# Optimization experiments

Measured on AMD Instinct MI355X. Metric: run time of the kernel, lower is better.

Reference implementation:

```python
import jax, jax.numpy as jnp
import numpy as np

V, D, NL, K, B, L, FF = 32000, 512, 4, 32, 2, 1024, 2048


def _ln(x, g, b, eps=1e-5):
    m = jnp.mean(x, axis=-1, keepdims=True)
    v = jnp.mean((x - m) ** 2, axis=-1, keepdims=True)
    return (x - m) * jax.lax.rsqrt(v + eps) * g + b


def setup_inputs() -> dict:
    key = jax.random.key(0)
    ks = jax.random.split(key, 16)
    s = 0.02
    n = lambda k, shape: jax.random.normal(k, shape, jnp.float32) * s
    inp = {
        "tokens": jax.random.randint(ks[0], (B, L), 0, V),
        "embed": n(ks[1], (V, D)),
        "ln1_g": jnp.ones((NL, D)), "ln1_b": jnp.zeros((NL, D)),
        "cp_w1": n(ks[2], (NL, D, D)), "cp_b1": jnp.zeros((NL, D)),
        "cp_w2": n(ks[3], (NL, D, K)), "cp_b2": jnp.zeros((NL, K)),
        "pos_scale": 0.5 * jnp.ones((NL,)), "content_scale": 0.5 * jnp.ones((NL,)),
        "val_w": n(ks[4], (NL, D, D)), "val_b": jnp.zeros((NL, D)),
        "oln_g": jnp.ones((NL, D)), "oln_b": jnp.zeros((NL, D)),
        "out_w": n(ks[5], (NL, D, D)), "out_b": jnp.zeros((NL, D)),
        "ln2_g": jnp.ones((NL, D)), "ln2_b": jnp.zeros((NL, D)),
        "ffn_w1": n(ks[6], (NL, D, FF)), "ffn_b1": jnp.zeros((NL, FF)),
        "ffn_w2": n(ks[7], (NL, FF, D)), "ffn_b2": jnp.zeros((NL, D)),
        "no_g": jnp.ones((D,)), "no_b": jnp.zeros((D,)),
        "head_b": jnp.zeros((V,)),
    }
    return inp


def _forward(tokens, embed, ln1_g, ln1_b, cp_w1, cp_b1, cp_w2, cp_b2,
             pos_scale, content_scale, val_w, val_b, oln_g, oln_b, out_w, out_b,
             ln2_g, ln2_b, ffn_w1, ffn_b1, ffn_w2, ffn_b2, no_g, no_b, head_b):
    Bn, Ln = tokens.shape
    Kn = cp_b2.shape[1]
    # fixed positional phases (register_buffer in torch)
    freqs = 1.0 / 10000.0 ** (jnp.arange(Kn, dtype=jnp.float32) / Kn)
    pos_phase = jnp.arange(Ln, dtype=jnp.float32)[:, None] * freqs[None, :]  # [L,K]
    inv_norm = 1.0 / jnp.sqrt(jnp.arange(1, Ln + 1, dtype=jnp.float32) * Kn)[None, :, None]
    h = embed[tokens]  # [B,L,D]
    for i in range(ln1_g.shape[0]):
        # --- DualAddressingPhasor on normed input ---
        x = _ln(h, ln1_g[i], ln1_b[i])
        cp = jnp.tanh(jnp.tanh(x @ cp_w1[i] + cp_b1[i]) @ cp_w2[i] + cp_b2[i]) * jnp.pi  # [B,L,K]
        tp = pos_scale[i] * pos_phase[None] + content_scale[i] * cp
        v = x @ val_w[i] + val_b[i]  # [B,L,D]
        c, s_ = jnp.cos(tp), jnp.sin(tp)  # [B,L,K]
        mem_r = jnp.cumsum(c[..., None] * v[:, :, None, :], axis=1)  # [B,L,K,D]
        mem_i = jnp.cumsum(s_[..., None] * v[:, :, None, :], axis=1)
        retrieved = (jnp.einsum('blkd,blk->bld', mem_r, c)
                     + jnp.einsum('blkd,blk->bld', mem_i, s_)) * inv_norm
        # phasor returns x + to_out(retrieved); block adds it back to h
        h = h + x + (_ln(retrieved, oln_g[i], oln_b[i]) @ out_w[i] + out_b[i])
        # --- FFN ---
        y = _ln(h, ln2_g[i], ln2_b[i])
        h = h + jax.nn.gelu(y @ ffn_w1[i] + ffn_b1[i], approximate=False) @ ffn_w2[i] + ffn_b2[i]
    # tied output head: head.weight = embed.weight
    return _ln(h, no_g, no_b) @ embed.T + head_b


def reference(tokens, embed, ln1_g, ln1_b, cp_w1, cp_b1, cp_w2, cp_b2,
              pos_scale, content_scale, val_w, val_b, oln_g, oln_b, out_w, out_b,
              ln2_g, ln2_b, ffn_w1, ffn_b1, ffn_w2, ffn_b2, no_g, no_b, head_b):
    return _forward(tokens, embed, ln1_g, ln1_b, cp_w1, cp_b1, cp_w2, cp_b2,
                    pos_scale, content_scale, val_w, val_b, oln_g, oln_b, out_w, out_b,
                    ln2_g, ln2_b, ffn_w1, ffn_b1, ffn_w2, ffn_b2, no_g, no_b, head_b)
```

## Files before the change

### kernel.cpp

```cpp
#include <hip/hip_runtime.h>
#include <hip/hip_bf16.h>
#include <math.h>

#define V_  32000
#define D_  512
#define NL_ 4
#define K_  32
#define B_  2
#define L_  1024
#define FF_ 2048
#define MR_ (B_ * L_)

typedef __bf16 bf16_t;
typedef __bf16 bf16x8 __attribute__((ext_vector_type(8)));
typedef float  f32x4  __attribute__((ext_vector_type(4)));

#define FLAG_TANH   1
#define FLAG_GELU   2
#define FLAG_INV    8
#define FLAG_CAUSAL 16
#define FLAG_TANHLO 32

#define GLDS(gsrc, ldst) \
  __builtin_amdgcn_global_load_lds( \
      (const __attribute__((address_space(1))) unsigned int*)(const void*)(gsrc), \
      (__attribute__((address_space(3))) unsigned int*)(void*)(ldst), 16, 0, 0)

__global__ void gather_kernel(const int* __restrict__ tokens,
                              const float* __restrict__ embed,
                              float* __restrict__ h) {
    int row = blockIdx.x;
    int t = tokens[row];
    const float4* src = (const float4*)(embed + (size_t)t * D_);
    float4* dst = (float4*)(h + (size_t)row * D_);
    dst[threadIdx.x] = src[threadIdx.x];
}

__global__ __launch_bounds__(256) void cvt_kernel(const float* __restrict__ in,
                                                  bf16_t* __restrict__ out) {
    size_t i = ((size_t)blockIdx.x * 256 + threadIdx.x) * 8;
    float4 f0 = ((const float4*)(in + i))[0];
    float4 f1 = ((const float4*)(in + i))[1];
    bf16x8 ov;
    ov[0] = (bf16_t)f0.x; ov[1] = (bf16_t)f0.y;
    ov[2] = (bf16_t)f0.z; ov[3] = (bf16_t)f0.w;
    ov[4] = (bf16_t)f1.x; ov[5] = (bf16_t)f1.y;
    ov[6] = (bf16_t)f1.z; ov[7] = (bf16_t)f1.w;
    *(bf16x8*)(out + i) = ov;
}

__global__ void bconcat_kernel(const float* __restrict__ a,
                               const float* __restrict__ b,
                               float* __restrict__ o) {
    int i = blockIdx.x, t = threadIdx.x;
    o[(size_t)i * 2 * D_ + t]       = a[(size_t)i * D_ + t];
    o[(size_t)i * 2 * D_ + D_ + t]  = b[(size_t)i * D_ + t];
}

__global__ __launch_bounds__(256) void ln_kernel(const float* __restrict__ in,
                                                 const float* __restrict__ g,
                                                 const float* __restrict__ b,
                                                 float* __restrict__ outf,
                                                 bf16_t* __restrict__ outb) {
    int row = blockIdx.x, tid = threadIdx.x;
    const float* rp = in + (size_t)row * D_;
    float v0 = rp[tid], v1 = rp[tid + 256];
    float s = v0 + v1, q = v0 * v0 + v1 * v1;
#pragma unroll
    for (int o = 32; o > 0; o >>= 1) {
        s += __shfl_down(s, o, 64);
        q += __shfl_down(q, o, 64);
    }
    __shared__ float ss[4], sq[4];
    if ((tid & 63) == 0) { ss[tid >> 6] = s; sq[tid >> 6] = q; }
    __syncthreads();
    float ts = ss[0] + ss[1] + ss[2] + ss[3];
    float tq = sq[0] + sq[1] + sq[2] + sq[3];
    float mean = ts * (1.0f / D_);
    float var = tq * (1.0f / D_) - mean * mean;
    float rstd = rsqrtf(var + 1e-5f);
    float o0 = (v0 - mean) * rstd * g[tid] + b[tid];
    float o1 = (v1 - mean) * rstd * g[tid + 256] + b[tid + 256];
    if (outf) {
        outf[(size_t)row * D_ + tid]       = o0;
        outf[(size_t)row * D_ + tid + 256] = o1;
    }
    if (outb) {
        outb[(size_t)row * D_ + tid]       = (bf16_t)o0;
        outb[(size_t)row * D_ + tid + 256] = (bf16_t)o1;
    }
}

__global__ __launch_bounds__(256) void tconv_kernel(const float* __restrict__ in,
                                                    bf16_t* __restrict__ out,
                                                    int R, int C,
                                                    size_t inz, size_t outz) {
    __shared__ float t[32][33];
    const float* ip = in + (size_t)blockIdx.z * inz;
    bf16_t* op = out + (size_t)blockIdx.z * outz;
    int r0 = blockIdx.y * 32, c0 = blockIdx.x * 32;
    int tx = threadIdx.x & 31, ty = threadIdx.x >> 5;
#pragma unroll
    for (int rr = 0; rr < 4; ++rr)
        t[ty + rr * 8][tx] = ip[(size_t)(r0 + ty + rr * 8) * C + c0 + tx];
    __syncthreads();
#pragma unroll
    for (int rr = 0; rr < 4; ++rr)
        op[(size_t)(c0 + ty + rr * 8) * R + r0 + tx] = (bf16_t)t[tx][ty + rr * 8];
}

template<int BM, int BN, int NBUF, bool BF32>
__global__ __launch_bounds__(256) void mgemm(
    const bf16_t* __restrict__ A, const void* __restrict__ Bp,
    const float* __restrict__ bias, const float* __restrict__ res1,
    const float* __restrict__ res2, float* __restrict__ Cf,
    bf16_t* __restrict__ Cb, int M, int N, int Kd, int flags,
    long long strA, long long strB, long long strC, int swz) {
    __shared__ bf16_t sA[NBUF][BM * 32];
    __shared__ bf16_t sB[NBUF][BN * 32];
    const int tid = threadIdx.x;
    const int wave = tid >> 6, lane = tid & 63;
    const int lrow = lane & 15, quad = lane >> 4;
    int bx = blockIdx.x, by = blockIdx.y;
    if (swz) {
        int gx = gridDim.x, gy = gridDim.y;
        int nwg = gx * gy;
        int lid = by * gx + bx;
        int q = nwg >> 3, r = nwg & 7;
        int xcd = lid & 7, slot = lid >> 3;
        int base = (xcd < r) ? xcd * (q + 1) : r * (q + 1) + (xcd - r) * q;
        int nid = base + slot;
        bx = nid / gy;
        by = nid - bx * gy;
    }
    const int m0 = by * BM, n0 = bx * BN;
    const int z = blockIdx.z;
    A += (size_t)z * strA;
    const bf16_t* Bb = (const bf16_t*)Bp + (BF32 ? 0 : (size_t)z * strB);
    const float*  Bf = (const float*)Bp  + (BF32 ? (size_t)z * strB : 0);
    constexpr int TM = BM / 32, TN = BN / 32;
    const int wm = (wave >> 1) * (BM / 2), wn = (wave & 1) * (BN / 2);
    f32x4 acc[TM][TN] = {};

    if constexpr (BF32) {
        for (int k0 = 0; k0 < Kd; k0 += 32) {
#pragma unroll
            for (int rb = 0; rb < BM / 64; ++rb) {
                int rowblk = wave * (BM / 64) + rb;
                int ml = rowblk * 16 + (lane >> 2);
                int qs = (lane & 3) ^ ((ml >> 1) & 3);
                GLDS(A + (size_t)(m0 + ml) * Kd + k0 + qs * 8, &sA[0][rowblk * 512]);
            }
#pragma unroll
            for (int rb = 0; rb < (BN * 4) / 256; ++rb) {
                int s = rb * 256 + tid;
                int nl = s >> 2, ql = s & 3;
                int qs = ql ^ ((nl >> 1) & 3);
                const float* src = Bf + (size_t)(n0 + nl) * Kd + k0 + qs * 8;
                float4 f0 = ((const float4*)src)[0];
                float4 f1 = ((const float4*)src)[1];
                bf16x8 ov;
                ov[0] = (bf16_t)f0.x; ov[1] = (bf16_t)f0.y;
                ov[2] = (bf16_t)f0.z; ov[3] = (bf16_t)f0.w;
                ov[4] = (bf16_t)f1.x; ov[5] = (bf16_t)f1.y;
                ov[6] = (bf16_t)f1.z; ov[7] = (bf16_t)f1.w;
                *(bf16x8*)(&sB[0][s * 8]) = ov;
            }
            __syncthreads();
            bf16x8 af[TM], bv[TN];
#pragma unroll
            for (int i = 0; i < TM; ++i) {
                int row = wm + i * 16 + lrow;
                af[i] = *(const bf16x8*)(&sA[0][(row * 4 + (quad ^ ((row >> 1) & 3))) * 8]);
            }
#pragma unroll
            for (int j = 0; j < TN; ++j) {
                int rown = wn + j * 16 + lrow;
                bv[j] = *(const bf16x8*)(&sB[0][(rown * 4 + (quad ^ ((rown >> 1) & 3))) * 8]);
            }
#pragma unroll
            for (int i = 0; i < TM; ++i)
#pragma unroll
                for (int j = 0; j < TN; ++j)
                    acc[i][j] = __builtin_amdgcn_mfma_f32_16x16x32_bf16(af[i], bv[j], acc[i][j], 0, 0, 0);
            __syncthreads();
        }
    } else {
        int kend = Kd;
        if (flags & FLAG_CAUSAL) { int ke = m0 + BM; kend = ke < Kd ? ke : Kd; }
        const int nk = kend >> 5;
        constexpr int NLD = BM / 64 + BN / 64;
        auto stage = [&](int t) {
            const int buf = t & (NBUF - 1);
            const int k0 = t << 5;
#pragma unroll
            for (int rb = 0; rb < BM / 64; ++rb) {
                int rowblk = wave * (BM / 64) + rb;
                int ml = rowblk * 16 + (lane >> 2);
                int qs = (lane & 3) ^ ((ml >> 1) & 3);
                GLDS(A + (size_t)(m0 + ml) * Kd + k0 + qs * 8, &sA[buf][rowblk * 512]);
            }
#pragma unroll
            for (int rb = 0; rb < BN / 64; ++rb) {
                int rowblk = wave * (BN / 64) + rb;
                int nl = rowblk * 16 + (lane >> 2);
                int qs = (lane & 3) ^ ((nl >> 1) & 3);
                GLDS(Bb + (size_t)(n0 + nl) * Kd + k0 + qs * 8, &sB[buf][rowblk * 512]);
            }
        };
        for (int t = 0; t < NBUF - 1 && t < nk; ++t) stage(t);
        for (int t = 0; t < nk; ++t) {
            const int nxt = t + NBUF - 1;
            if (nxt < nk) stage(nxt);
            const int issued_last = (nxt < nk) ? nxt : nk - 1;
            const int ahead = issued_last - t;
            switch (ahead) {
              case 0: asm volatile("s_waitcnt vmcnt(0)" ::: "memory"); break;
              case 1: asm volatile("s_waitcnt vmcnt(%0)" :: "n"(1 * NLD) : "memory"); break;
              case 2: asm volatile("s_waitcnt vmcnt(%0)" :: "n"(2 * NLD) : "memory"); break;
              default: asm volatile("s_waitcnt vmcnt(%0)" :: "n"(3 * NLD) : "memory"); break;
            }
            __builtin_amdgcn_s_barrier();
            const int buf = t & (NBUF - 1);
            const bf16_t* sAc = sA[buf];
            const bf16_t* sBc = sB[buf];
            bf16x8 af[TM], bv[TN];
#pragma unroll
            for (int i = 0; i < TM; ++i) {
                int row = wm + i * 16 + lrow;
                af[i] = *(const bf16x8*)(sAc + (row * 4 + (quad ^ ((row >> 1) & 3))) * 8);
            }
#pragma unroll
            for (int j = 0; j < TN; ++j) {
                int rown = wn + j * 16 + lrow;
                bv[j] = *(const bf16x8*)(sBc + (rown * 4 + (quad ^ ((rown >> 1) & 3))) * 8);
            }
#pragma unroll
            for (int i = 0; i < TM; ++i)
#pragma unroll
                for (int j = 0; j < TN; ++j)
                    acc[i][j] = __builtin_amdgcn_mfma_f32_16x16x32_bf16(af[i], bv[j], acc[i][j], 0, 0, 0);
            asm volatile("s_waitcnt lgkmcnt(0)" ::: "memory");
            __builtin_amdgcn_s_barrier();
        }
    }

    const size_t zo = (size_t)z * strC;
#pragma unroll
    for (int i = 0; i < TM; ++i) {
#pragma unroll
        for (int reg = 0; reg < 4; ++reg) {
            int m = m0 + wm + i * 16 + quad * 4 + reg;
            float rs = (flags & FLAG_INV) ? rsqrtf((float)(m + 1) * (float)K_) : 1.0f;
#pragma unroll
            for (int j = 0; j < TN; ++j) {
                int n = n0 + wn + j * 16 + lrow;
                float vv = acc[i][j][reg];
                if (bias) vv += bias[n];
                vv *= rs;
                if (flags & FLAG_TANH) vv = tanhf(vv);
                else if (flags & FLAG_GELU) vv = 0.5f * vv * (1.0f + erff(vv * 0.7071067811865476f));
                else if (flags & FLAG_TANHLO) { if (n < D_) vv = tanhf(vv); }
                size_t idx = zo + (size_t)m * N + n;
                if (res1) vv += res1[idx];
                if (res2) vv += res2[idx];
                if (Cf) Cf[idx] = vv;
                if (Cb) Cb[idx] = (bf16_t)vv;
            }
        }
    }
}

__global__ void phase_kernel(const float* __restrict__ t1,
                             const float* __restrict__ w2,
                             const float* __restrict__ b2,
                             const float* __restrict__ ps,
                             const float* __restrict__ cs,
                             int layer,
                             float* __restrict__ cbuf,
                             float* __restrict__ sbuf) {
    int row = blockIdx.x;
    int l = row & (L_ - 1);
    int tid = threadIdx.x;
    int k = tid & 31, hh = tid >> 5;
    const float* tr = t1 + (size_t)row * (2 * D_);
    float acc = 0.f;
    for (int d = hh * 256; d < hh * 256 + 256; ++d)
        acc = fmaf(tr[d], w2[d * K_ + k], acc);
    __shared__ float red[64];
    red[tid] = acc;
    __syncthreads();
    if (hh == 0) {
        float zz = red[k] + red[k + 32] + b2[k];
        float cp = tanhf(zz) * 3.14159265358979323846f;
        float freq = expf(-(float)k * (9.210340371976184f / (float)K_));
        float tp = ps[layer] * (float)l * freq + cs[layer] * cp;
        cbuf[(size_t)row * K_ + k] = cosf(tp);
        sbuf[(size_t)row * K_ + k] = sinf(tp);
    }
}

__global__ __launch_bounds__(256) void score_kernel(const float* __restrict__ cbuf,
                                                    const float* __restrict__ sbuf,
                                                    bf16_t* __restrict__ Ab) {
    int b = blockIdx.z;
    int l0 = blockIdx.y * 16, j0 = blockIdx.x * 16;
    if (j0 > l0) return;
    int tx = threadIdx.x, ty = threadIdx.y;
    int tid = ty * 16 + tx;
    __shared__ float Cl[16][33], Sl[16][33], Cj[16][33], Sj[16][33];
    const float* cb = cbuf + (size_t)b * L_ * K_;
    const float* sb = sbuf + (size_t)b * L_ * K_;
    for (int q = tid; q < 16 * 32; q += 256) {
        int rr = q >> 5, kk = q & 31;
        Cl[rr][kk] = cb[(size_t)(l0 + rr) * K_ + kk];
        Sl[rr][kk] = sb[(size_t)(l0 + rr) * K_ + kk];
        Cj[rr][kk] = cb[(size_t)(j0 + rr) * K_ + kk];
        Sj[rr][kk] = sb[(size_t)(j0 + rr) * K_ + kk];
    }
    __syncthreads();
    int l = l0 + ty, j = j0 + tx;
    float acc = 0.f;
#pragma unroll
    for (int kk = 0; kk < 32; ++kk)
        acc += Cl[ty][kk] * Cj[tx][kk] + Sl[ty][kk] * Sj[tx][kk];
    Ab[((size_t)b * L_ + l) * L_ + j] = (bf16_t)((j <= l) ? acc : 0.f);
}

extern "C" void kernel_launch(void* const* d_in, const int* in_sizes, int n_in,
                              void* d_out, int out_size, void* d_ws, size_t ws_size,
                              hipStream_t stream) {
    const int*   tokens        = (const int*)d_in[0];
    const float* embed         = (const float*)d_in[1];
    const float* ln1_g         = (const float*)d_in[2];
    const float* ln1_b         = (const float*)d_in[3];
    const float* cp_w1         = (const float*)d_in[4];
    const float* cp_b1         = (const float*)d_in[5];
    const float* cp_w2         = (const float*)d_in[6];
    const float* cp_b2         = (const float*)d_in[7];
    const float* pos_scale     = (const float*)d_in[8];
    const float* content_scale = (const float*)d_in[9];
    const float* val_w         = (const float*)d_in[10];
    const float* val_b         = (const float*)d_in[11];
    const float* oln_g         = (const float*)d_in[12];
    const float* oln_b         = (const float*)d_in[13];
    const float* out_w         = (const float*)d_in[14];
    const float* out_b         = (const float*)d_in[15];
    const float* ln2_g         = (const float*)d_in[16];
    const float* ln2_b         = (const float*)d_in[17];
    const float* ffn_w1        = (const float*)d_in[18];
    const float* ffn_b1        = (const float*)d_in[19];
    const float* ffn_w2        = (const float*)d_in[20];
    const float* ffn_b2        = (const float*)d_in[21];
    const float* no_g          = (const float*)d_in[22];
    const float* no_b          = (const float*)d_in[23];
    const float* head_b        = (const float*)d_in[24];
    float* out = (float*)d_out;

    float* h   = out;
    float* x   = h  + (size_t)MR_ * D_;
    float* t1v = x  + (size_t)MR_ * D_;
    float* r   = t1v + (size_t)MR_ * 2 * D_;
    float* cb  = r  + (size_t)MR_ * D_;
    float* sb  = cb + (size_t)MR_ * K_;
    bf16_t* x_bf  = (bf16_t*)(sb + (size_t)MR_ * K_);
    bf16_t* r_bf  = x_bf  + (size_t)MR_ * D_;
    bf16_t* y_bf  = r_bf  + (size_t)MR_ * D_;
    bf16_t* ff_bf = y_bf  + (size_t)MR_ * D_;
    bf16_t* sc_bf = ff_bf + (size_t)MR_ * FF_;
    bf16_t* vT_bf = sc_bf + (size_t)B_ * L_ * L_;
    bf16_t* wvT   = vT_bf + (size_t)B_ * D_ * L_;
    bf16_t* owT   = wvT   + (size_t)NL_ * 2 * D_ * D_;
    bf16_t* f1T   = owT   + (size_t)NL_ * D_ * D_;
    bf16_t* f2T   = f1T   + (size_t)NL_ * FF_ * D_;
    float*  b1v   = (float*)((((uintptr_t)(f2T + (size_t)NL_ * D_ * FF_)) + 15) & ~(uintptr_t)15);
    bf16_t* hn_bf = (bf16_t*)d_ws;
    bf16_t* emb_bf = hn_bf + (size_t)MR_ * D_;
    const bool big_ws =
        ws_size >= ((size_t)MR_ * D_ + (size_t)V_ * D_) * sizeof(bf16_t);

    gather_kernel<<<MR_, 128, 0, stream>>>(tokens, embed, h);

    tconv_kernel<<<dim3(16, 16, NL_), 256, 0, stream>>>(cp_w1, wvT, D_, D_, (size_t)D_ * D_, (size_t)2 * D_ * D_);
    tconv_kernel<<<dim3(16, 16, NL_), 256, 0, stream>>>(val_w, wvT + (size_t)D_ * D_, D_, D_, (size_t)D_ * D_, (size_t)2 * D_ * D_);
    bconcat_kernel<<<NL_, 512, 0, stream>>>(cp_b1, val_b, b1v);
    tconv_kernel<<<dim3(16, 16, NL_), 256, 0, stream>>>(out_w, owT, D_, D_, (size_t)D_ * D_, (size_t)D_ * D_);
    tconv_kernel<<<dim3(64, 16, NL_), 256, 0, stream>>>(ffn_w1, f1T, D_, FF_, (size_t)D_ * FF_, (size_t)D_ * FF_);
    tconv_kernel<<<dim3(16, 64, NL_), 256, 0, stream>>>(ffn_w2, f2T, FF_, D_, (size_t)FF_ * D_, (size_t)FF_ * D_);
    if (big_ws)
        cvt_kernel<<<(V_ * D_) / 2048, 256, 0, stream>>>(embed, emb_bf);

    for (int i = 0; i < NL_; ++i) {
        ln_kernel<<<MR_, 256, 0, stream>>>(h, ln1_g + i * D_, ln1_b + i * D_, x, x_bf);
        mgemm<64, 64, 4, false><<<dim3(16, 32, 1), 256, 0, stream>>>(
            x_bf, wvT + (size_t)i * 2 * D_ * D_, b1v + (size_t)i * 2 * D_,
            nullptr, nullptr, t1v, nullptr, MR_, 2 * D_, D_, FLAG_TANHLO, 0, 0, 0, 1);
        phase_kernel<<<MR_, 64, 0, stream>>>(
            t1v, cp_w2 + (size_t)i * D_ * K_, cp_b2 + i * K_,
            pos_scale, content_scale, i, cb, sb);
        tconv_kernel<<<dim3(16, 32, B_), 256, 0, stream>>>(
            t1v + D_, vT_bf, L_, 2 * D_, (size_t)L_ * 2 * D_, (size_t)D_ * L_);
        score_kernel<<<dim3(L_ / 16, L_ / 16, B_), dim3(16, 16), 0, stream>>>(cb, sb, sc_bf);
        mgemm<64, 64, 4, false><<<dim3(8, 16, B_), 256, 0, stream>>>(
            sc_bf, vT_bf, nullptr, nullptr, nullptr, r, nullptr,
            L_, D_, L_, FLAG_INV | FLAG_CAUSAL,
            (long long)L_ * L_, (long long)D_ * L_, (long long)L_ * D_, 1);
        ln_kernel<<<MR_, 256, 0, stream>>>(r, oln_g + i * D_, oln_b + i * D_, nullptr, r_bf);
        mgemm<64, 64, 4, false><<<dim3(8, 32, 1), 256, 0, stream>>>(
            r_bf, owT + (size_t)i * D_ * D_, out_b + i * D_,
            h, x, h, nullptr, MR_, D_, D_, 0, 0, 0, 0, 1);
        ln_kernel<<<MR_, 256, 0, stream>>>(h, ln2_g + i * D_, ln2_b + i * D_, nullptr, y_bf);
        mgemm<128, 128, 4, false><<<dim3(16, 16, 1), 256, 0, stream>>>(
            y_bf, f1T + (size_t)i * FF_ * D_, ffn_b1 + i * FF_,
            nullptr, nullptr, nullptr, ff_bf, MR_, FF_, D_, FLAG_GELU, 0, 0, 0, 1);
        mgemm<64, 64, 4, false><<<dim3(8, 32, 1), 256, 0, stream>>>(
            ff_bf, f2T + (size_t)i * D_ * FF_, ffn_b2 + i * D_,
            h, nullptr, h, nullptr, MR_, D_, FF_, 0, 0, 0, 0, 1);
    }

    ln_kernel<<<MR_, 256, 0, stream>>>(h, no_g, no_b, nullptr, hn_bf);
    if (big_ws) {
        mgemm<128, 128, 2, false><<<dim3(V_ / 128, MR_ / 128, 1), 256, 0, stream>>>(
            hn_bf, emb_bf, head_b, nullptr, nullptr, out, nullptr,
            MR_, V_, D_, 0, 0, 0, 0, 1);
    } else {
        mgemm<128, 128, 1, true><<<dim3(V_ / 128, MR_ / 128, 1), 256, 0, stream>>>(
            hn_bf, embed, head_b, nullptr, nullptr, out, nullptr,
            MR_, V_, D_, 0, 0, 0, 0, 1);
    }
}
```

Baseline: 1.508 ms.

## Load GEMM operands straight to registers, compute scores with MFMA, retune tiles

```diff
diff --git a/kernel.cpp b/kernel.cpp
--- a/kernel.cpp
+++ b/kernel.cpp
@@ -20,6 +20,7 @@
 #define FLAG_INV    8
 #define FLAG_CAUSAL 16
 #define FLAG_TANHLO 32
+#define FLAG_TRI    64
 
 #define GLDS(gsrc, ldst) \
   __builtin_amdgcn_global_load_lds( \
@@ -109,15 +110,13 @@
         op[(size_t)(c0 + ty + rr * 8) * R + r0 + tx] = (bf16_t)t[tx][ty + rr * 8];
 }
 
-template<int BM, int BN, int NBUF, bool BF32>
+template<int BM, int BN, bool BF32>
 __global__ __launch_bounds__(256) void mgemm(
     const bf16_t* __restrict__ A, const void* __restrict__ Bp,
     const float* __restrict__ bias, const float* __restrict__ res1,
     const float* __restrict__ res2, float* __restrict__ Cf,
     bf16_t* __restrict__ Cb, int M, int N, int Kd, int flags,
     long long strA, long long strB, long long strC, int swz) {
-    __shared__ bf16_t sA[NBUF][BM * 32];
-    __shared__ bf16_t sB[NBUF][BN * 32];
     const int tid = threadIdx.x;
     const int wave = tid >> 6, lane = tid & 63;
     const int lrow = lane & 15, quad = lane >> 4;
@@ -133,6 +132,7 @@
         bx = nid / gy;
         by = nid - bx * gy;
     }
+    if (flags & FLAG_TRI) { if (bx > by) return; }
     const int m0 = by * BM, n0 = bx * BN;
     const int z = blockIdx.z;
     A += (size_t)z * strA;
@@ -143,13 +143,15 @@
     f32x4 acc[TM][TN] = {};
 
     if constexpr (BF32) {
+        __shared__ bf16_t sA[BM * 32];
+        __shared__ bf16_t sB[BN * 32];
         for (int k0 = 0; k0 < Kd; k0 += 32) {
 #pragma unroll
             for (int rb = 0; rb < BM / 64; ++rb) {
                 int rowblk = wave * (BM / 64) + rb;
                 int ml = rowblk * 16 + (lane >> 2);
                 int qs = (lane & 3) ^ ((ml >> 1) & 3);
-                GLDS(A + (size_t)(m0 + ml) * Kd + k0 + qs * 8, &sA[0][rowblk * 512]);
+                GLDS(A + (size_t)(m0 + ml) * Kd + k0 + qs * 8, &sA[rowblk * 512]);
             }
 #pragma unroll
             for (int rb = 0; rb < (BN * 4) / 256; ++rb) {
@@ -164,19 +166,19 @@
                 ov[2] = (bf16_t)f0.z; ov[3] = (bf16_t)f0.w;
                 ov[4] = (bf16_t)f1.x; ov[5] = (bf16_t)f1.y;
                 ov[6] = (bf16_t)f1.z; ov[7] = (bf16_t)f1.w;
-                *(bf16x8*)(&sB[0][s * 8]) = ov;
+                *(bf16x8*)(&sB[s * 8]) = ov;
             }
             __syncthreads();
             bf16x8 af[TM], bv[TN];
 #pragma unroll
             for (int i = 0; i < TM; ++i) {
                 int row = wm + i * 16 + lrow;
-                af[i] = *(const bf16x8*)(&sA[0][(row * 4 + (quad ^ ((row >> 1) & 3))) * 8]);
+                af[i] = *(const bf16x8*)(&sA[(row * 4 + (quad ^ ((row >> 1) & 3))) * 8]);
             }
 #pragma unroll
             for (int j = 0; j < TN; ++j) {
                 int rown = wn + j * 16 + lrow;
-                bv[j] = *(const bf16x8*)(&sB[0][(rown * 4 + (quad ^ ((rown >> 1) & 3))) * 8]);
+                bv[j] = *(const bf16x8*)(&sB[(rown * 4 + (quad ^ ((rown >> 1) & 3))) * 8]);
             }
 #pragma unroll
             for (int i = 0; i < TM; ++i)
@@ -189,59 +191,51 @@
         int kend = Kd;
         if (flags & FLAG_CAUSAL) { int ke = m0 + BM; kend = ke < Kd ? ke : Kd; }
         const int nk = kend >> 5;
-        constexpr int NLD = BM / 64 + BN / 64;
-        auto stage = [&](int t) {
-            const int buf = t & (NBUF - 1);
-            const int k0 = t << 5;
-#pragma unroll
-            for (int rb = 0; rb < BM / 64; ++rb) {
-                int rowblk = wave * (BM / 64) + rb;
-                int ml = rowblk * 16 + (lane >> 2);
-                int qs = (lane & 3) ^ ((ml >> 1) & 3);
-                GLDS(A + (size_t)(m0 + ml) * Kd + k0 + qs * 8, &sA[buf][rowblk * 512]);
-            }
-#pragma unroll
-            for (int rb = 0; rb < BN / 64; ++rb) {
-                int rowblk = wave * (BN / 64) + rb;
-                int nl = rowblk * 16 + (lane >> 2);
-                int qs = (lane & 3) ^ ((nl >> 1) & 3);
-                GLDS(Bb + (size_t)(n0 + nl) * Kd + k0 + qs * 8, &sB[buf][rowblk * 512]);
-            }
+        const bf16_t* aP[TM];
+        const bf16_t* bP[TN];
+#pragma unroll
+        for (int i = 0; i < TM; ++i)
+            aP[i] = A + (size_t)(m0 + wm + i * 16 + lrow) * Kd + quad * 8;
+#pragma unroll
+        for (int j = 0; j < TN; ++j)
+            bP[j] = Bb + (size_t)(n0 + wn + j * 16 + lrow) * Kd + quad * 8;
+
+        bf16x8 a0[TM], b0[TN], a1[TM], b1[TN];
+        auto load0 = [&](int t) {
+            const int kb = t << 5;
+#pragma unroll
+            for (int i = 0; i < TM; ++i) a0[i] = *(const bf16x8*)(aP[i] + kb);
+#pragma unroll
+            for (int j = 0; j < TN; ++j) b0[j] = *(const bf16x8*)(bP[j] + kb);
         };
-        for (int t = 0; t < NBUF - 1 && t < nk; ++t) stage(t);
-        for (int t = 0; t < nk; ++t) {
-            const int nxt = t + NBUF - 1;
-            if (nxt < nk) stage(nxt);
-            const int issued_last = (nxt < nk) ? nxt : nk - 1;
-            const int ahead = issued_last - t;
-            switch (ahead) {
-              case 0: asm volatile("s_waitcnt vmcnt(0)" ::: "memory"); break;
-              case 1: asm volatile("s_waitcnt vmcnt(%0)" :: "n"(1 * NLD) : "memory"); break;
-              case 2: asm volatile("s_waitcnt vmcnt(%0)" :: "n"(2 * NLD) : "memory"); break;
-              default: asm volatile("s_waitcnt vmcnt(%0)" :: "n"(3 * NLD) : "memory"); break;
-            }
-            __builtin_amdgcn_s_barrier();
-            const int buf = t & (NBUF - 1);
-            const bf16_t* sAc = sA[buf];
-            const bf16_t* sBc = sB[buf];
-            bf16x8 af[TM], bv[TN];
-#pragma unroll
-            for (int i = 0; i < TM; ++i) {
-                int row = wm + i * 16 + lrow;
-                af[i] = *(const bf16x8*)(sAc + (row * 4 + (quad ^ ((row >> 1) & 3))) * 8);
-            }
-#pragma unroll
-            for (int j = 0; j < TN; ++j) {
-                int rown = wn + j * 16 + lrow;
-                bv[j] = *(const bf16x8*)(sBc + (rown * 4 + (quad ^ ((rown >> 1) & 3))) * 8);
-            }
+        auto load1 = [&](int t) {
+            const int kb = t << 5;
+#pragma unroll
+            for (int i = 0; i < TM; ++i) a1[i] = *(const bf16x8*)(aP[i] + kb);
+#pragma unroll
+            for (int j = 0; j < TN; ++j) b1[j] = *(const bf16x8*)(bP[j] + kb);
+        };
+        auto domfma0 = [&]() {
 #pragma unroll
             for (int i = 0; i < TM; ++i)
 #pragma unroll
                 for (int j = 0; j < TN; ++j)
-                    acc[i][j] = __builtin_amdgcn_mfma_f32_16x16x32_bf16(af[i], bv[j], acc[i][j], 0, 0, 0);
-            asm volatile("s_waitcnt lgkmcnt(0)" ::: "memory");
-            __builtin_amdgcn_s_barrier();
+                    acc[i][j] = __builtin_amdgcn_mfma_f32_16x16x32_bf16(a0[i], b0[j], acc[i][j], 0, 0, 0);
+        };
+        auto domfma1 = [&]() {
+#pragma unroll
+            for (int i = 0; i < TM; ++i)
+#pragma unroll
+                for (int j = 0; j < TN; ++j)
+                    acc[i][j] = __builtin_amdgcn_mfma_f32_16x16x32_bf16(a1[i], b1[j], acc[i][j], 0, 0, 0);
+        };
+
+        load0(0);
+        for (int t = 0; t < nk; t += 2) {
+            load1(t + 1);
+            domfma0();
+            if (t + 2 < nk) load0(t + 2);
+            domfma1();
         }
     }
 
@@ -261,6 +255,7 @@
                 if (flags & FLAG_TANH) vv = tanhf(vv);
                 else if (flags & FLAG_GELU) vv = 0.5f * vv * (1.0f + erff(vv * 0.7071067811865476f));
                 else if (flags & FLAG_TANHLO) { if (n < D_) vv = tanhf(vv); }
+                if ((flags & FLAG_TRI) && n > m) vv = 0.f;
                 size_t idx = zo + (size_t)m * N + n;
                 if (res1) vv += res1[idx];
                 if (res2) vv += res2[idx];
@@ -277,8 +272,7 @@
                              const float* __restrict__ ps,
                              const float* __restrict__ cs,
                              int layer,
-                             float* __restrict__ cbuf,
-                             float* __restrict__ sbuf) {
+                             bf16_t* __restrict__ csb) {
     int row = blockIdx.x;
     int l = row & (L_ - 1);
     int tid = threadIdx.x;
@@ -295,36 +289,9 @@
         float cp = tanhf(zz) * 3.14159265358979323846f;
         float freq = expf(-(float)k * (9.210340371976184f / (float)K_));
         float tp = ps[layer] * (float)l * freq + cs[layer] * cp;
-        cbuf[(size_t)row * K_ + k] = cosf(tp);
-        sbuf[(size_t)row * K_ + k] = sinf(tp);
-    }
-}
-
-__global__ __launch_bounds__(256) void score_kernel(const float* __restrict__ cbuf,
-                                                    const float* __restrict__ sbuf,
-                                                    bf16_t* __restrict__ Ab) {
-    int b = blockIdx.z;
-    int l0 = blockIdx.y * 16, j0 = blockIdx.x * 16;
-    if (j0 > l0) return;
-    int tx = threadIdx.x, ty = threadIdx.y;
-    int tid = ty * 16 + tx;
-    __shared__ float Cl[16][33], Sl[16][33], Cj[16][33], Sj[16][33];
-    const float* cb = cbuf + (size_t)b * L_ * K_;
-    const float* sb = sbuf + (size_t)b * L_ * K_;
-    for (int q = tid; q < 16 * 32; q += 256) {
-        int rr = q >> 5, kk = q & 31;
-        Cl[rr][kk] = cb[(size_t)(l0 + rr) * K_ + kk];
-        Sl[rr][kk] = sb[(size_t)(l0 + rr) * K_ + kk];
-        Cj[rr][kk] = cb[(size_t)(j0 + rr) * K_ + kk];
-        Sj[rr][kk] = sb[(size_t)(j0 + rr) * K_ + kk];
-    }
-    __syncthreads();
-    int l = l0 + ty, j = j0 + tx;
-    float acc = 0.f;
-#pragma unroll
-    for (int kk = 0; kk < 32; ++kk)
-        acc += Cl[ty][kk] * Cj[tx][kk] + Sl[ty][kk] * Sj[tx][kk];
-    Ab[((size_t)b * L_ + l) * L_ + j] = (bf16_t)((j <= l) ? acc : 0.f);
+        csb[(size_t)row * 64 + k]      = (bf16_t)cosf(tp);
+        csb[(size_t)row * 64 + 32 + k] = (bf16_t)sinf(tp);
+    }
 }
 
 extern "C" void kernel_launch(void* const* d_in, const int* in_sizes, int n_in,
@@ -361,19 +328,18 @@
     float* x   = h  + (size_t)MR_ * D_;
     float* t1v = x  + (size_t)MR_ * D_;
     float* r   = t1v + (size_t)MR_ * 2 * D_;
-    float* cb  = r  + (size_t)MR_ * D_;
-    float* sb  = cb + (size_t)MR_ * K_;
-    bf16_t* x_bf  = (bf16_t*)(sb + (size_t)MR_ * K_);
+    bf16_t* x_bf  = (bf16_t*)(r + (size_t)MR_ * D_);
     bf16_t* r_bf  = x_bf  + (size_t)MR_ * D_;
     bf16_t* y_bf  = r_bf  + (size_t)MR_ * D_;
     bf16_t* ff_bf = y_bf  + (size_t)MR_ * D_;
     bf16_t* sc_bf = ff_bf + (size_t)MR_ * FF_;
     bf16_t* vT_bf = sc_bf + (size_t)B_ * L_ * L_;
-    bf16_t* wvT   = vT_bf + (size_t)B_ * D_ * L_;
+    bf16_t* csb   = vT_bf + (size_t)B_ * D_ * L_;
+    bf16_t* wvT   = csb   + (size_t)MR_ * 64;
     bf16_t* owT   = wvT   + (size_t)NL_ * 2 * D_ * D_;
     bf16_t* f1T   = owT   + (size_t)NL_ * D_ * D_;
     bf16_t* f2T   = f1T   + (size_t)NL_ * FF_ * D_;
-    float*  b1v   = (float*)((((uintptr_t)(f2T + (size_t)NL_ * D_ * FF_)) + 15) & ~(uintptr_t)15);
+    float*  b1v   = (float*)(f2T + (size_t)NL_ * D_ * FF_);
     bf16_t* hn_bf = (bf16_t*)d_ws;
     bf16_t* emb_bf = hn_bf + (size_t)MR_ * D_;
     const bool big_ws =
@@ -392,39 +358,42 @@
 
     for (int i = 0; i < NL_; ++i) {
         ln_kernel<<<MR_, 256, 0, stream>>>(h, ln1_g + i * D_, ln1_b + i * D_, x, x_bf);
-        mgemm<64, 64, 4, false><<<dim3(16, 32, 1), 256, 0, stream>>>(
+        mgemm<64, 64, false><<<dim3(16, 32, 1), 256, 0, stream>>>(
             x_bf, wvT + (size_t)i * 2 * D_ * D_, b1v + (size_t)i * 2 * D_,
             nullptr, nullptr, t1v, nullptr, MR_, 2 * D_, D_, FLAG_TANHLO, 0, 0, 0, 1);
         phase_kernel<<<MR_, 64, 0, stream>>>(
             t1v, cp_w2 + (size_t)i * D_ * K_, cp_b2 + i * K_,
-            pos_scale, content_scale, i, cb, sb);
+            pos_scale, content_scale, i, csb);
         tconv_kernel<<<dim3(16, 32, B_), 256, 0, stream>>>(
             t1v + D_, vT_bf, L_, 2 * D_, (size_t)L_ * 2 * D_, (size_t)D_ * L_);
-        score_kernel<<<dim3(L_ / 16, L_ / 16, B_), dim3(16, 16), 0, stream>>>(cb, sb, sc_bf);
-        mgemm<64, 64, 4, false><<<dim3(8, 16, B_), 256, 0, stream>>>(
+        mgemm<64, 64, false><<<dim3(L_ / 64, L_ / 64, B_), 256, 0, stream>>>(
+            csb, csb, nullptr, nullptr, nullptr, nullptr, sc_bf,
+            L_, L_, 64, FLAG_TRI,
+            (long long)L_ * 64, (long long)L_ * 64, (long long)L_ * L_, 0);
+        mgemm<64, 32, false><<<dim3(16, 16, B_), 256, 0, stream>>>(
             sc_bf, vT_bf, nullptr, nullptr, nullptr, r, nullptr,
             L_, D_, L_, FLAG_INV | FLAG_CAUSAL,
             (long long)L_ * L_, (long long)D_ * L_, (long long)L_ * D_, 1);
         ln_kernel<<<MR_, 256, 0, stream>>>(r, oln_g + i * D_, oln_b + i * D_, nullptr, r_bf);
-        mgemm<64, 64, 4, false><<<dim3(8, 32, 1), 256, 0, stream>>>(
+        mgemm<64, 32, false><<<dim3(16, 32, 1), 256, 0, stream>>>(
             r_bf, owT + (size_t)i * D_ * D_, out_b + i * D_,
             h, x, h, nullptr, MR_, D_, D_, 0, 0, 0, 0, 1);
         ln_kernel<<<MR_, 256, 0, stream>>>(h, ln2_g + i * D_, ln2_b + i * D_, nullptr, y_bf);
-        mgemm<128, 128, 4, false><<<dim3(16, 16, 1), 256, 0, stream>>>(
+        mgemm<64, 64, false><<<dim3(32, 32, 1), 256, 0, stream>>>(
             y_bf, f1T + (size_t)i * FF_ * D_, ffn_b1 + i * FF_,
             nullptr, nullptr, nullptr, ff_bf, MR_, FF_, D_, FLAG_GELU, 0, 0, 0, 1);
-        mgemm<64, 64, 4, false><<<dim3(8, 32, 1), 256, 0, stream>>>(
+        mgemm<64, 32, false><<<dim3(16, 32, 1), 256, 0, stream>>>(
             ff_bf, f2T + (size_t)i * D_ * FF_, ffn_b2 + i * D_,
             h, nullptr, h, nullptr, MR_, D_, FF_, 0, 0, 0, 0, 1);
     }
 
     ln_kernel<<<MR_, 256, 0, stream>>>(h, no_g, no_b, nullptr, hn_bf);
     if (big_ws) {
-        mgemm<128, 128, 2, false><<<dim3(V_ / 128, MR_ / 128, 1), 256, 0, stream>>>(
+        mgemm<128, 128, false><<<dim3(V_ / 128, MR_ / 128, 1), 256, 0, stream>>>(
             hn_bf, emb_bf, head_b, nullptr, nullptr, out, nullptr,
             MR_, V_, D_, 0, 0, 0, 0, 1);
     } else {
-        mgemm<128, 128, 1, true><<<dim3(V_ / 128, MR_ / 128, 1), 256, 0, stream>>>(
+        mgemm<128, 128, true><<<dim3(V_ / 128, MR_ / 128, 1), 256, 0, stream>>>(
             hn_bf, embed, head_b, nullptr, nullptr, out, nullptr,
             MR_, V_, D_, 0, 0, 0, 0, 1);
     }
```

Measured after the change: 1.788 ms. 1.19x slower.
